# Performance work log

Hardware: AMD Instinct MI355X
Metric: run time of the kernel (lower is better)

Reference implementation:

```python
import jax, jax.numpy as jnp
import numpy as np

N_NODES = 50000
N_EDGES = 800000
D = 128
N_LAYERS = 4


def _sage_conv(x, edge_index, Wl, bl, Wr):
    # PyG SAGEConv (mean aggr): out = lin_l(mean_{j in N(i)} x_j) + lin_r(x_i)
    src, dst = edge_index[0], edge_index[1]
    msgs = x[src]                                            # [E, D] gather
    summed = jax.ops.segment_sum(msgs, dst, num_segments=N_NODES)   # [N, D]
    cnt = jax.ops.segment_sum(jnp.ones((msgs.shape[0],), x.dtype), dst,
                              num_segments=N_NODES)
    mean = summed / jnp.maximum(cnt, 1.0)[:, None]           # [N, D]
    return mean @ Wl.T + bl + x @ Wr.T


def setup_inputs() -> dict:
    key = jax.random.key(0)
    ks = jax.random.split(key, 2 + 3 * N_LAYERS)
    x = jax.random.normal(ks[0], (N_NODES, D), dtype=jnp.float32)
    edge_index = jax.random.randint(ks[1], (2, N_EDGES), 0, N_NODES, dtype=jnp.int64)
    inp = {"x": x, "edge_index": edge_index}
    s = 1.0 / np.sqrt(D)
    for i in range(N_LAYERS):
        inp[f"Wl{i}"] = jax.random.uniform(ks[2 + 3 * i], (D, D), jnp.float32, -s, s)
        inp[f"bl{i}"] = jax.random.uniform(ks[3 + 3 * i], (D,), jnp.float32, -s, s)
        inp[f"Wr{i}"] = jax.random.uniform(ks[4 + 3 * i], (D, D), jnp.float32, -s, s)
    return inp


def reference(x, edge_index, Wl0, bl0, Wr0, Wl1, bl1, Wr1, Wl2, bl2, Wr2, Wl3, bl3, Wr3):
    # ReLU only after the first conv, per the original forward.
    h = jax.nn.relu(_sage_conv(x, edge_index, Wl0, bl0, Wr0))
    h = _sage_conv(h, edge_index, Wl1, bl1, Wr1)
    h = _sage_conv(h, edge_index, Wl2, bl2, Wr2)
    h = _sage_conv(h, edge_index, Wl3, bl3, Wr3)
    return h
```

## Files before the change

kernel.cpp:

```cpp
#include <hip/hip_runtime.h>
#include <stdint.h>

#define NN 50000
#define NE 800000
#define NB 196
#define CAST_B 6250
#define CVTW_B 512
#define CNT_B 3125

typedef short short8 __attribute__((ext_vector_type(8)));
typedef float f32x4 __attribute__((ext_vector_type(4)));
typedef unsigned int uint;
typedef unsigned short ushort;

__device__ __forceinline__ uint rne_bf16(float f) {
    uint x = __float_as_uint(f);
    return (x + 0x7FFFu + ((x >> 16) & 1u)) >> 16;
}
__device__ __forceinline__ float bf_lo(uint d) { return __uint_as_float(d << 16); }
__device__ __forceinline__ float bf_hi(uint d) { return __uint_as_float(d & 0xFFFF0000u); }

__device__ __forceinline__ int ei_is64(const int* __restrict__ ei) {
    return (ei[1] | ei[3] | ei[5] | ei[7]) == 0;
}

struct Ptrs8 { const float* p[8]; };

__global__ __launch_bounds__(256) void k_prep(
    const float* __restrict__ x, ushort* __restrict__ xbf, Ptrs8 ps,
    ushort* __restrict__ wbf, const int* __restrict__ ei,
    int* __restrict__ deg, ushort* __restrict__ rank) {
    int b = blockIdx.x;
    if (b < CAST_B) {
        int i = b * 256 + threadIdx.x;
        float4 v = ((const float4*)x)[i];
        uint2 o;
        o.x = rne_bf16(v.x) | (rne_bf16(v.y) << 16);
        o.y = rne_bf16(v.z) | (rne_bf16(v.w) << 16);
        ((uint2*)xbf)[i] = o;
    } else if (b < CAST_B + CVTW_B) {
        int idx = (b - CAST_B) * 256 + threadIdx.x;
        int m = idx >> 14;
        int off = idx & 16383;
        wbf[idx] = (ushort)rne_bf16(ps.p[m][off]);
    } else {
        int e = (b - CAST_B - CVTW_B) * 256 + threadIdx.x;
        int is64 = ei_is64(ei);
        int d = is64 ? ei[2 * NE + 2 * e] : ei[NE + e];
        int rk = atomicAdd(&deg[d], 1);
        rank[e] = (ushort)rk;
    }
}

__global__ __launch_bounds__(256) void k_blocksum(const int* __restrict__ deg,
                                                  int* __restrict__ bsum) {
    __shared__ int s[256];
    int i = blockIdx.x * 256 + threadIdx.x;
    s[threadIdx.x] = (i < NN) ? deg[i] : 0;
    __syncthreads();
    for (int off = 128; off > 0; off >>= 1) {
        if (threadIdx.x < off) s[threadIdx.x] += s[threadIdx.x + off];
        __syncthreads();
    }
    if (threadIdx.x == 0) bsum[blockIdx.x] = s[0];
}

__global__ __launch_bounds__(256) void k_scanb(const int* __restrict__ bsum,
                                               int* __restrict__ boff) {
    __shared__ int s[256];
    int t = threadIdx.x;
    s[t] = (t < NB) ? bsum[t] : 0;
    __syncthreads();
    for (int off = 1; off < 256; off <<= 1) {
        int v = s[t];
        int a = (t >= off) ? s[t - off] : 0;
        __syncthreads();
        s[t] = v + a;
        __syncthreads();
    }
    if (t < NB) boff[t] = (t == 0) ? 0 : s[t - 1];
}

__global__ __launch_bounds__(256) void k_writeptr(const int* __restrict__ deg,
                                                  const int* __restrict__ boff,
                                                  int* __restrict__ row_ptr,
                                                  float* __restrict__ rinv) {
    __shared__ int s[256];
    int b = blockIdx.x, t = threadIdx.x;
    int i = b * 256 + t;
    int d = (i < NN) ? deg[i] : 0;
    s[t] = d;
    __syncthreads();
    for (int off = 1; off < 256; off <<= 1) {
        int v = s[t];
        int a = (t >= off) ? s[t - off] : 0;
        __syncthreads();
        s[t] = v + a;
        __syncthreads();
    }
    if (i < NN) {
        int pos = boff[b] + s[t] - d;
        row_ptr[i] = pos;
        rinv[i] = 1.0f / (float)max(d, 1);
    }
    if (b == 0 && t == 0) row_ptr[NN] = NE;
}

__global__ void k_fill(const int* __restrict__ ei,
                       const int* __restrict__ row_ptr,
                       const ushort* __restrict__ rank, ushort* __restrict__ col) {
    int e = blockIdx.x * 256 + threadIdx.x;
    if (e >= NE) return;
    int is64 = ei_is64(ei);
    int sv = is64 ? ei[2 * e] : ei[e];
    int dv = is64 ? ei[2 * NE + 2 * e] : ei[NE + e];
    int p = row_ptr[dv] + (int)rank[e];
    col[p] = (ushort)sv;
}

__global__ __launch_bounds__(256) void k_agg3(const ushort* __restrict__ h,
                                              const int* __restrict__ row_ptr,
                                              const ushort* __restrict__ col,
                                              const float* __restrict__ rinv,
                                              ushort* __restrict__ mean) {
    int node = blockIdx.x * 4 + (threadIdx.x >> 6);
    if (node >= NN) return;
    int lane = threadIdx.x & 63;
    int beg = row_ptr[node], end = row_ptr[node + 1];
    const uint* hp = (const uint*)h;
    float a0 = 0.f, a1 = 0.f;
    for (int b = beg; b < end; b += 64) {
        int n = min(64, end - b);
        int c = (int)col[b + min(lane, n - 1)];
        for (int j0 = 0; j0 < n; j0 += 8) {
#pragma unroll
            for (int j = 0; j < 8; j++) {
                int jj = j0 + j;
                int s = __shfl(c, min(jj, n - 1));
                uint v = hp[s * 64 + lane];
                float m = (jj < n) ? 1.f : 0.f;
                a0 = fmaf(m, bf_lo(v), a0);
                a1 = fmaf(m, bf_hi(v), a1);
            }
        }
    }
    float r = rinv[node];
    ((uint*)mean)[node * 64 + lane] = rne_bf16(a0 * r) | (rne_bf16(a1 * r) << 16);
}

__global__ __launch_bounds__(256) void k_gemm_mfma(
    const ushort* __restrict__ Am, const ushort* __restrict__ Ah,
    const ushort* __restrict__ Wlb, const ushort* __restrict__ Wrb,
    const float* __restrict__ bias, float* __restrict__ outf,
    ushort* __restrict__ outb, int relu) {
    const int lane = threadIdx.x & 63;
    const int wave = threadIdx.x >> 6;
    const int l15 = lane & 15;
    const int quad = lane >> 4;
    const int m0 = blockIdx.x * 64 + wave * 16;

    f32x4 acc[8];
#pragma unroll
    for (int t = 0; t < 8; t++) acc[t] = (f32x4){0.f, 0.f, 0.f, 0.f};

    int arow = min(m0 + l15, NN - 1);
    const ushort* Arm = Am + (size_t)arow * 128 + quad * 8;
    const ushort* Arh = Ah + (size_t)arow * 128 + quad * 8;
    const int wro = quad * 8;

#pragma unroll
    for (int half = 0; half < 2; half++) {
        const ushort* Ar = half ? Arh : Arm;
        const ushort* W = half ? Wrb : Wlb;
#pragma unroll
        for (int k0 = 0; k0 < 128; k0 += 32) {
            short8 a = *(const short8*)(Ar + k0);
#pragma unroll
            for (int t = 0; t < 8; t++) {
                short8 b = *(const short8*)(W + (size_t)(t * 16 + l15) * 128 + k0 + wro);
                acc[t] = __builtin_amdgcn_mfma_f32_16x16x32_bf16(a, b, acc[t], 0, 0, 0);
            }
        }
    }

    float bb[8];
#pragma unroll
    for (int t = 0; t < 8; t++) bb[t] = bias[t * 16 + l15];

#pragma unroll
    for (int r = 0; r < 4; r++) {
        int row = m0 + quad * 4 + r;
        if (row < NN) {
#pragma unroll
            for (int t = 0; t < 8; t++) {
                float v = acc[t][r] + bb[t];
                if (relu) v = fmaxf(v, 0.f);
                if (outb) outb[(size_t)row * 128 + t * 16 + l15] = (ushort)rne_bf16(v);
                else outf[(size_t)row * 128 + t * 16 + l15] = v;
            }
        }
    }
}

extern "C" void kernel_launch(void* const* d_in, const int* in_sizes, int n_in,
                              void* d_out, int out_size, void* d_ws, size_t ws_size,
                              hipStream_t stream) {
    const float* x = (const float*)d_in[0];
    const int* ei = (const int*)d_in[1];
    const float* Wl[4] = {(const float*)d_in[2], (const float*)d_in[5],
                          (const float*)d_in[8], (const float*)d_in[11]};
    const float* bl[4] = {(const float*)d_in[3], (const float*)d_in[6],
                          (const float*)d_in[9], (const float*)d_in[12]};
    const float* Wr[4] = {(const float*)d_in[4], (const float*)d_in[7],
                          (const float*)d_in[10], (const float*)d_in[13]};
    float* out = (float*)d_out;

    char* p = (char*)d_ws;
    auto take = [&](size_t bytes) -> char* {
        char* r = p;
        p += (bytes + 255) & ~(size_t)255;
        return r;
    };
    int* deg = (int*)take(NN * 4);
    int* row_ptr = (int*)take((NN + 1) * 4);
    float* rinv = (float*)take(NN * 4);
    int* bsum = (int*)take(NB * 4);
    int* boff = (int*)take(NB * 4);
    ushort* rank = (ushort*)take((size_t)NE * 2);
    ushort* col = (ushort*)take((size_t)NE * 2 + 256);
    ushort* xbf = (ushort*)take((size_t)NN * 128 * 2);
    ushort* h1 = (ushort*)take((size_t)NN * 128 * 2);
    ushort* h2 = (ushort*)take((size_t)NN * 128 * 2);
    ushort* meanbf = (ushort*)take((size_t)NN * 128 * 2);
    ushort* wbf = (ushort*)take(8 * 16384 * 2);

    Ptrs8 ps;
    ps.p[0] = Wl[0]; ps.p[1] = Wr[0]; ps.p[2] = Wl[1]; ps.p[3] = Wr[1];
    ps.p[4] = Wl[2]; ps.p[5] = Wr[2]; ps.p[6] = Wl[3]; ps.p[7] = Wr[3];

    hipMemsetAsync(deg, 0, NN * 4, stream);
    k_prep<<<CAST_B + CVTW_B + CNT_B, 256, 0, stream>>>(x, xbf, ps, wbf, ei, deg,
                                                        rank);
    k_blocksum<<<NB, 256, 0, stream>>>(deg, bsum);
    k_scanb<<<1, 256, 0, stream>>>(bsum, boff);
    k_writeptr<<<NB, 256, 0, stream>>>(deg, boff, row_ptr, rinv);
    k_fill<<<CNT_B, 256, 0, stream>>>(ei, row_ptr, rank, col);

    const ushort* h = xbf;
    ushort* houts[4] = {h1, h2, h1, nullptr};
    for (int l = 0; l < 4; l++) {
        k_agg3<<<(NN + 3) / 4, 256, 0, stream>>>(h, row_ptr, col, rinv, meanbf);
        k_gemm_mfma<<<(NN + 63) / 64, 256, 0, stream>>>(
            meanbf, h, wbf + (size_t)(2 * l) * 16384,
            wbf + (size_t)(2 * l + 1) * 16384, bl[l], out, houts[l],
            l == 0 ? 1 : 0);
        h = houts[l];
    }
}
```

Before: 418.8 us.

## Privatize degree-count atomics per XCC with workgroup-scope histograms

Degree counting now uses one histogram per XCC, selected by reading the hardware XCC id, instead of a single global counter array. The atomics drop to workgroup scope, which is meant to keep them inside the XCC's own L2 and avoid cross-XCC coherent atomic traffic. A scan over the per-XCC slices then builds per-XCC row bases, and the fill step packs the XCC id into the rank word. The cost is a larger memset, wider rank storage and extra histogram passes. Correctness also depends on workgroup-scope atomics staying coherent between workgroups on the same XCC.

```diff
diff --git a/kernel.cpp b/kernel.cpp
--- a/kernel.cpp
+++ b/kernel.cpp
@@ -7,6 +7,7 @@
 #define CAST_B 6250
 #define CVTW_B 512
 #define CNT_B 3125
+#define NX 8
 
 typedef short short8 __attribute__((ext_vector_type(8)));
 typedef float f32x4 __attribute__((ext_vector_type(4)));
@@ -24,12 +25,18 @@
     return (ei[1] | ei[3] | ei[5] | ei[7]) == 0;
 }
 
+__device__ __forceinline__ int xcc_id() {
+    int x;
+    asm volatile("s_getreg_b32 %0, hwreg(HW_REG_XCC_ID, 0, 32)" : "=s"(x));
+    return x & (NX - 1);
+}
+
 struct Ptrs8 { const float* p[8]; };
 
 __global__ __launch_bounds__(256) void k_prep(
     const float* __restrict__ x, ushort* __restrict__ xbf, Ptrs8 ps,
     ushort* __restrict__ wbf, const int* __restrict__ ei,
-    int* __restrict__ deg, ushort* __restrict__ rank) {
+    int* __restrict__ hist, uint* __restrict__ rank) {
     int b = blockIdx.x;
     if (b < CAST_B) {
         int i = b * 256 + threadIdx.x;
@@ -47,16 +54,32 @@
         int e = (b - CAST_B - CVTW_B) * 256 + threadIdx.x;
         int is64 = ei_is64(ei);
         int d = is64 ? ei[2 * NE + 2 * e] : ei[NE + e];
-        int rk = atomicAdd(&deg[d], 1);
-        rank[e] = (ushort)rk;
-    }
-}
-
-__global__ __launch_bounds__(256) void k_blocksum(const int* __restrict__ deg,
+        int cid = xcc_id();
+        int rk = __hip_atomic_fetch_add(&hist[cid * NN + d], 1,
+                                        __ATOMIC_RELAXED,
+                                        __HIP_MEMORY_SCOPE_WORKGROUP);
+        rank[e] = (uint)rk | ((uint)cid << 16);
+    }
+}
+
+__global__ __launch_bounds__(256) void k_blocksum(int* __restrict__ hist,
+                                                  int* __restrict__ deg,
                                                   int* __restrict__ bsum) {
     __shared__ int s[256];
     int i = blockIdx.x * 256 + threadIdx.x;
-    s[threadIdx.x] = (i < NN) ? deg[i] : 0;
+    int sum = 0;
+    if (i < NN) {
+        int run = 0;
+#pragma unroll
+        for (int c = 0; c < NX; c++) {
+            int t = hist[c * NN + i];
+            hist[c * NN + i] = run;
+            run += t;
+        }
+        deg[i] = run;
+        sum = run;
+    }
+    s[threadIdx.x] = sum;
     __syncthreads();
     for (int off = 128; off > 0; off >>= 1) {
         if (threadIdx.x < off) s[threadIdx.x] += s[threadIdx.x + off];
@@ -83,7 +106,9 @@
 
 __global__ __launch_bounds__(256) void k_writeptr(const int* __restrict__ deg,
                                                   const int* __restrict__ boff,
+                                                  const int* __restrict__ hist,
                                                   int* __restrict__ row_ptr,
+                                                  int* __restrict__ rowb,
                                                   float* __restrict__ rinv) {
     __shared__ int s[256];
     int b = blockIdx.x, t = threadIdx.x;
@@ -102,19 +127,22 @@
         int pos = boff[b] + s[t] - d;
         row_ptr[i] = pos;
         rinv[i] = 1.0f / (float)max(d, 1);
+#pragma unroll
+        for (int c = 0; c < NX; c++) rowb[c * NN + i] = pos + hist[c * NN + i];
     }
     if (b == 0 && t == 0) row_ptr[NN] = NE;
 }
 
 __global__ void k_fill(const int* __restrict__ ei,
-                       const int* __restrict__ row_ptr,
-                       const ushort* __restrict__ rank, ushort* __restrict__ col) {
+                       const int* __restrict__ rowb,
+                       const uint* __restrict__ rank, ushort* __restrict__ col) {
     int e = blockIdx.x * 256 + threadIdx.x;
     if (e >= NE) return;
     int is64 = ei_is64(ei);
     int sv = is64 ? ei[2 * e] : ei[e];
     int dv = is64 ? ei[2 * NE + 2 * e] : ei[NE + e];
-    int p = row_ptr[dv] + (int)rank[e];
+    uint r = rank[e];
+    int p = rowb[(int)(r >> 16) * NN + dv] + (int)(r & 0xFFFFu);
     col[p] = (ushort)sv;
 }
 
@@ -221,12 +249,14 @@
         p += (bytes + 255) & ~(size_t)255;
         return r;
     };
+    int* hist = (int*)take((size_t)NX * NN * 4);
     int* deg = (int*)take(NN * 4);
     int* row_ptr = (int*)take((NN + 1) * 4);
+    int* rowb = (int*)take((size_t)NX * NN * 4);
     float* rinv = (float*)take(NN * 4);
     int* bsum = (int*)take(NB * 4);
     int* boff = (int*)take(NB * 4);
-    ushort* rank = (ushort*)take((size_t)NE * 2);
+    uint* rank = (uint*)take((size_t)NE * 4);
     ushort* col = (ushort*)take((size_t)NE * 2 + 256);
     ushort* xbf = (ushort*)take((size_t)NN * 128 * 2);
     ushort* h1 = (ushort*)take((size_t)NN * 128 * 2);
@@ -238,13 +268,13 @@
     ps.p[0] = Wl[0]; ps.p[1] = Wr[0]; ps.p[2] = Wl[1]; ps.p[3] = Wr[1];
     ps.p[4] = Wl[2]; ps.p[5] = Wr[2]; ps.p[6] = Wl[3]; ps.p[7] = Wr[3];
 
-    hipMemsetAsync(deg, 0, NN * 4, stream);
-    k_prep<<<CAST_B + CVTW_B + CNT_B, 256, 0, stream>>>(x, xbf, ps, wbf, ei, deg,
-                                                        rank);
-    k_blocksum<<<NB, 256, 0, stream>>>(deg, bsum);
+    hipMemsetAsync(hist, 0, (size_t)NX * NN * 4, stream);
+    k_prep<<<CAST_B + CVTW_B + CNT_B, 256, 0, stream>>>(x, xbf, ps, wbf, ei,
+                                                        hist, rank);
+    k_blocksum<<<NB, 256, 0, stream>>>(hist, deg, bsum);
     k_scanb<<<1, 256, 0, stream>>>(bsum, boff);
-    k_writeptr<<<NB, 256, 0, stream>>>(deg, boff, row_ptr, rinv);
-    k_fill<<<CNT_B, 256, 0, stream>>>(ei, row_ptr, rank, col);
+    k_writeptr<<<NB, 256, 0, stream>>>(deg, boff, hist, row_ptr, rowb, rinv);
+    k_fill<<<CNT_B, 256, 0, stream>>>(ei, rowb, rank, col);
 
     const ushort* h = xbf;
     ushort* houts[4] = {h1, h2, h1, nullptr};
```

Result: no change. 418.7 us (-0.0%).

## Build CSR with two-pass block-local radix sort instead of global atomic counting

Applied to the files above, without the earlier changes.

Replaces the global-atomic degree count, three-kernel scan and rank-based fill with a two-level bucket sort. Edges are packed as (dst<<16|src), histogrammed into 196 coarse buckets in shared memory, then scattered and sorted within each bucket by the low 8 dst bits. The goal is to remove contended global atomics and the memset plus several launches. The per-node reciprocal degree is now computed inline in the aggregation kernel. In exchange it adds extra edge-buffer traffic, and the 1024-thread sort blocks only see modest per-bucket parallelism.

```diff
diff --git a/kernel.cpp b/kernel.cpp
--- a/kernel.cpp
+++ b/kernel.cpp
@@ -3,10 +3,11 @@
 
 #define NN 50000
 #define NE 800000
-#define NB 196
 #define CAST_B 6250
 #define CVTW_B 512
-#define CNT_B 3125
+#define EPB 8192
+#define HIST_B 98
+#define NBK 196
 
 typedef short short8 __attribute__((ext_vector_type(8)));
 typedef float f32x4 __attribute__((ext_vector_type(4)));
@@ -29,7 +30,8 @@
 __global__ __launch_bounds__(256) void k_prep(
     const float* __restrict__ x, ushort* __restrict__ xbf, Ptrs8 ps,
     ushort* __restrict__ wbf, const int* __restrict__ ei,
-    int* __restrict__ deg, ushort* __restrict__ rank) {
+    uint* __restrict__ ebuf, int* __restrict__ hcnt) {
+    __shared__ int hs[NBK];
     int b = blockIdx.x;
     if (b < CAST_B) {
         int i = b * 256 + threadIdx.x;
@@ -44,32 +46,36 @@
         int off = idx & 16383;
         wbf[idx] = (ushort)rne_bf16(ps.p[m][off]);
     } else {
-        int e = (b - CAST_B - CVTW_B) * 256 + threadIdx.x;
+        int hb = b - CAST_B - CVTW_B;
+        int t = threadIdx.x;
+        for (int i = t; i < NBK; i += 256) hs[i] = 0;
+        __syncthreads();
+        int base = hb * EPB;
         int is64 = ei_is64(ei);
-        int d = is64 ? ei[2 * NE + 2 * e] : ei[NE + e];
-        int rk = atomicAdd(&deg[d], 1);
-        rank[e] = (ushort)rk;
-    }
-}
-
-__global__ __launch_bounds__(256) void k_blocksum(const int* __restrict__ deg,
-                                                  int* __restrict__ bsum) {
-    __shared__ int s[256];
-    int i = blockIdx.x * 256 + threadIdx.x;
-    s[threadIdx.x] = (i < NN) ? deg[i] : 0;
-    __syncthreads();
-    for (int off = 128; off > 0; off >>= 1) {
-        if (threadIdx.x < off) s[threadIdx.x] += s[threadIdx.x + off];
-        __syncthreads();
-    }
-    if (threadIdx.x == 0) bsum[blockIdx.x] = s[0];
-}
-
-__global__ __launch_bounds__(256) void k_scanb(const int* __restrict__ bsum,
-                                               int* __restrict__ boff) {
+        for (int i = 0; i < EPB; i += 256) {
+            int e = base + i + t;
+            if (e < NE) {
+                int sv = is64 ? ei[2 * e] : ei[e];
+                int dv = is64 ? ei[2 * NE + 2 * e] : ei[NE + e];
+                ebuf[e] = ((uint)dv << 16) | (uint)sv;
+                atomicAdd(&hs[dv >> 8], 1);
+            }
+        }
+        __syncthreads();
+        for (int i = t; i < NBK; i += 256) hcnt[hb * NBK + i] = hs[i];
+    }
+}
+
+__global__ __launch_bounds__(256) void k_scan1(const int* __restrict__ hcnt,
+                                               int* __restrict__ hoff,
+                                               int* __restrict__ bb,
+                                               int* __restrict__ row_ptr) {
     __shared__ int s[256];
     int t = threadIdx.x;
-    s[t] = (t < NB) ? bsum[t] : 0;
+    int tot = 0;
+    if (t < NBK)
+        for (int b = 0; b < HIST_B; b++) tot += hcnt[b * NBK + t];
+    s[t] = tot;
     __syncthreads();
     for (int off = 1; off < 256; off <<= 1) {
         int v = s[t];
@@ -78,50 +84,73 @@
         s[t] = v + a;
         __syncthreads();
     }
-    if (t < NB) boff[t] = (t == 0) ? 0 : s[t - 1];
-}
-
-__global__ __launch_bounds__(256) void k_writeptr(const int* __restrict__ deg,
-                                                  const int* __restrict__ boff,
-                                                  int* __restrict__ row_ptr,
-                                                  float* __restrict__ rinv) {
-    __shared__ int s[256];
-    int b = blockIdx.x, t = threadIdx.x;
-    int i = b * 256 + t;
-    int d = (i < NN) ? deg[i] : 0;
-    s[t] = d;
+    if (t < NBK) {
+        int base = (t == 0) ? 0 : s[t - 1];
+        bb[t] = base;
+        int run = base;
+        for (int b = 0; b < HIST_B; b++) {
+            hoff[b * NBK + t] = run;
+            run += hcnt[b * NBK + t];
+        }
+    }
+    if (t == 0) { bb[NBK] = NE; row_ptr[NN] = NE; }
+}
+
+__global__ __launch_bounds__(256) void k_scatter1(const uint* __restrict__ ebuf,
+                                                  const int* __restrict__ hoff,
+                                                  uint* __restrict__ ebuf2) {
+    __shared__ int pos[NBK];
+    int hb = blockIdx.x, t = threadIdx.x;
+    for (int i = t; i < NBK; i += 256) pos[i] = hoff[hb * NBK + i];
+    __syncthreads();
+    int base = hb * EPB;
+    for (int i = 0; i < EPB; i += 256) {
+        int e = base + i + t;
+        if (e < NE) {
+            uint pk = ebuf[e];
+            int idx = atomicAdd(&pos[pk >> 24], 1);
+            ebuf2[idx] = pk;
+        }
+    }
+}
+
+__global__ __launch_bounds__(1024) void k_sort2(const uint* __restrict__ ebuf2,
+                                                const int* __restrict__ bb,
+                                                int* __restrict__ row_ptr,
+                                                ushort* __restrict__ col) {
+    __shared__ int hist[256];
+    __shared__ int pos[256];
+    int k = blockIdx.x, t = threadIdx.x;
+    int beg = bb[k], end = bb[k + 1];
+    if (t < 256) hist[t] = 0;
+    __syncthreads();
+    for (int j = beg + t; j < end; j += 1024)
+        atomicAdd(&hist[(ebuf2[j] >> 16) & 255], 1);
     __syncthreads();
     for (int off = 1; off < 256; off <<= 1) {
-        int v = s[t];
-        int a = (t >= off) ? s[t - off] : 0;
-        __syncthreads();
-        s[t] = v + a;
-        __syncthreads();
-    }
-    if (i < NN) {
-        int pos = boff[b] + s[t] - d;
-        row_ptr[i] = pos;
-        rinv[i] = 1.0f / (float)max(d, 1);
-    }
-    if (b == 0 && t == 0) row_ptr[NN] = NE;
-}
-
-__global__ void k_fill(const int* __restrict__ ei,
-                       const int* __restrict__ row_ptr,
-                       const ushort* __restrict__ rank, ushort* __restrict__ col) {
-    int e = blockIdx.x * 256 + threadIdx.x;
-    if (e >= NE) return;
-    int is64 = ei_is64(ei);
-    int sv = is64 ? ei[2 * e] : ei[e];
-    int dv = is64 ? ei[2 * NE + 2 * e] : ei[NE + e];
-    int p = row_ptr[dv] + (int)rank[e];
-    col[p] = (ushort)sv;
+        int v = 0;
+        if (t < 256) { v = hist[t]; if (t >= off) v += hist[t - off]; }
+        __syncthreads();
+        if (t < 256) hist[t] = v;
+        __syncthreads();
+    }
+    if (t < 256) {
+        int ex = (t == 0) ? 0 : hist[t - 1];
+        pos[t] = beg + ex;
+        int node = k * 256 + t;
+        if (node < NN) row_ptr[node] = beg + ex;
+    }
+    __syncthreads();
+    for (int j = beg + t; j < end; j += 1024) {
+        uint pk = ebuf2[j];
+        int idx = atomicAdd(&pos[(pk >> 16) & 255], 1);
+        col[idx] = (ushort)(pk & 0xFFFFu);
+    }
 }
 
 __global__ __launch_bounds__(256) void k_agg3(const ushort* __restrict__ h,
                                               const int* __restrict__ row_ptr,
                                               const ushort* __restrict__ col,
-                                              const float* __restrict__ rinv,
                                               ushort* __restrict__ mean) {
     int node = blockIdx.x * 4 + (threadIdx.x >> 6);
     if (node >= NN) return;
@@ -144,7 +173,7 @@
             }
         }
     }
-    float r = rinv[node];
+    float r = 1.0f / (float)max(end - beg, 1);
     ((uint*)mean)[node * 64 + lane] = rne_bf16(a0 * r) | (rne_bf16(a1 * r) << 16);
 }
 
@@ -221,12 +250,12 @@
         p += (bytes + 255) & ~(size_t)255;
         return r;
     };
-    int* deg = (int*)take(NN * 4);
+    uint* ebuf = (uint*)take((size_t)NE * 4);
+    uint* ebuf2 = (uint*)take((size_t)NE * 4);
+    int* hcnt = (int*)take((size_t)HIST_B * NBK * 4);
+    int* hoff = (int*)take((size_t)HIST_B * NBK * 4);
+    int* bb = (int*)take((NBK + 1) * 4);
     int* row_ptr = (int*)take((NN + 1) * 4);
-    float* rinv = (float*)take(NN * 4);
-    int* bsum = (int*)take(NB * 4);
-    int* boff = (int*)take(NB * 4);
-    ushort* rank = (ushort*)take((size_t)NE * 2);
     ushort* col = (ushort*)take((size_t)NE * 2 + 256);
     ushort* xbf = (ushort*)take((size_t)NN * 128 * 2);
     ushort* h1 = (ushort*)take((size_t)NN * 128 * 2);
@@ -238,18 +267,16 @@
     ps.p[0] = Wl[0]; ps.p[1] = Wr[0]; ps.p[2] = Wl[1]; ps.p[3] = Wr[1];
     ps.p[4] = Wl[2]; ps.p[5] = Wr[2]; ps.p[6] = Wl[3]; ps.p[7] = Wr[3];
 
-    hipMemsetAsync(deg, 0, NN * 4, stream);
-    k_prep<<<CAST_B + CVTW_B + CNT_B, 256, 0, stream>>>(x, xbf, ps, wbf, ei, deg,
-                                                        rank);
-    k_blocksum<<<NB, 256, 0, stream>>>(deg, bsum);
-    k_scanb<<<1, 256, 0, stream>>>(bsum, boff);
-    k_writeptr<<<NB, 256, 0, stream>>>(deg, boff, row_ptr, rinv);
-    k_fill<<<CNT_B, 256, 0, stream>>>(ei, row_ptr, rank, col);
+    k_prep<<<CAST_B + CVTW_B + HIST_B, 256, 0, stream>>>(x, xbf, ps, wbf, ei,
+                                                         ebuf, hcnt);
+    k_scan1<<<1, 256, 0, stream>>>(hcnt, hoff, bb, row_ptr);
+    k_scatter1<<<HIST_B, 256, 0, stream>>>(ebuf, hoff, ebuf2);
+    k_sort2<<<NBK, 1024, 0, stream>>>(ebuf2, bb, row_ptr, col);
 
     const ushort* h = xbf;
     ushort* houts[4] = {h1, h2, h1, nullptr};
     for (int l = 0; l < 4; l++) {
-        k_agg3<<<(NN + 3) / 4, 256, 0, stream>>>(h, row_ptr, col, rinv, meanbf);
+        k_agg3<<<(NN + 3) / 4, 256, 0, stream>>>(h, row_ptr, col, meanbf);
         k_gemm_mfma<<<(NN + 63) / 64, 256, 0, stream>>>(
             meanbf, h, wbf + (size_t)(2 * l) * 16384,
             wbf + (size_t)(2 * l + 1) * 16384, bl[l], out, houts[l],
```

Result: faster. 406.3 us (-3.0%).
